# Optimization experiments

Measured on AMD Instinct MI355X. Metric: run time of the kernel, lower is better.

Reference implementation:

```python
import jax, jax.numpy as jnp
import numpy as np

VOCAB, VEC, HID, ATT, DOM, B, S = 50000, 300, 256, 500, 16, 64, 128


def _gru_scan(gi_all, h0, Whh, bhh):
    # gi_all: [S,B,3H] precomputed input projections; returns hs: [S,B,H]
    def step(h, gi):
        gh = h @ Whh.T + bhh
        i_r, i_z, i_n = jnp.split(gi, 3, axis=-1)
        h_r, h_z, h_n = jnp.split(gh, 3, axis=-1)
        r = jax.nn.sigmoid(i_r + h_r)
        zg = jax.nn.sigmoid(i_z + h_z)
        n = jnp.tanh(i_n + r * h_n)
        h_new = (1.0 - zg) * n + zg * h
        return h_new, h_new
    _, hs = jax.lax.scan(step, h0, gi_all)
    return hs


def setup_inputs() -> dict:
    key = jax.random.key(0)
    ks = jax.random.split(key, 16)
    def xavier(k, shape):
        fan_in, fan_out = shape[-1], shape[0]
        std = float(np.sqrt(2.0 / (fan_in + fan_out)))
        return jax.random.normal(k, shape, dtype=jnp.float32) * std
    inp = {
        'x': jax.random.randint(ks[0], (B, S), 0, VOCAB),
        'z': jax.random.randint(ks[1], (B,), 0, DOM),
        'emb': jax.random.normal(ks[2], (VOCAB, VEC), dtype=jnp.float32) * 0.1,
        'Wih_f': xavier(ks[3], (3 * HID, VEC)),
        'Whh_f': xavier(ks[4], (3 * HID, HID)),
        'bih_f': jnp.zeros((3 * HID,), jnp.float32),
        'bhh_f': jnp.zeros((3 * HID,), jnp.float32),
        'Wih_b': xavier(ks[5], (3 * HID, VEC)),
        'Whh_b': xavier(ks[6], (3 * HID, HID)),
        'bih_b': jnp.zeros((3 * HID,), jnp.float32),
        'bhh_b': jnp.zeros((3 * HID,), jnp.float32),
        'att_fc_W': xavier(ks[7], (ATT, 2 * HID)),
        'att_fc_b': jnp.zeros((ATT,), jnp.float32),
        'att_weight': xavier(ks[8], (DOM, ATT)),
        'fc_W': xavier(ks[9], (2, 2 * HID)),
        'fc_b': jnp.zeros((2,), jnp.float32),
    }
    return inp


def reference(x, z, emb, Wih_f, Whh_f, bih_f, bhh_f, Wih_b, Whh_b, bih_b, bhh_b,
              att_fc_W, att_fc_b, att_weight, fc_W, fc_b):
    xe = emb[x]                              # [B,S,VEC]
    xs = jnp.transpose(xe, (1, 0, 2))        # [S,B,VEC] (seq-major like torch GRU)
    h0 = jnp.zeros((x.shape[0], HID), jnp.float32)
    gi_f = jnp.einsum('sbv,gv->sbg', xs, Wih_f) + bih_f
    hs_f = _gru_scan(gi_f, h0, Whh_f, bhh_f)                       # [S,B,H]
    gi_b = jnp.einsum('sbv,gv->sbg', xs[::-1], Wih_b) + bih_b
    hs_b = _gru_scan(gi_b, h0, Whh_b, bhh_b)[::-1]                 # [S,B,H]
    h = jnp.transpose(jnp.concatenate([hs_f, hs_b], axis=-1), (1, 0, 2))  # [B,S,2H]
    hr = jnp.tanh(jnp.einsum('bsh,ah->bsa', h, att_fc_W) + att_fc_b)      # [B,S,ATT]
    # batched gather of per-domain attention vector, then per-row dot
    u = jnp.einsum('bsa,ba->bs', hr, att_weight[z])                        # [B,S]
    att = jax.nn.softmax(u, axis=1)                                        # [B,S]
    pooled = jnp.einsum('bsh,bs->bh', h, att)                              # [B,2H]
    # dropout is identity in eval mode
    return pooled @ fc_W.T + fc_b                                          # [B,2]
```

## Files before the change

### kernel.cpp

```cpp
#include <hip/hip_runtime.h>
#include <math.h>

#define VEC   300
#define HID   256
#define ATT   500
#define NB    64
#define NS    128
#define G3    768
#define GIC   1536
#define H2    512

typedef _Float16 half1;
typedef _Float16 h2_t  __attribute__((ext_vector_type(2)));
typedef _Float16 f16x8 __attribute__((ext_vector_type(8)));
typedef float    f32x4 __attribute__((ext_vector_type(4)));

struct __align__(16) H8 { h2_t a, b, c, d; };

#if __has_builtin(__builtin_amdgcn_exp2f)
#define EXP2F(x) __builtin_amdgcn_exp2f(x)
#else
#define EXP2F(x) exp2f(x)
#endif
#if __has_builtin(__builtin_amdgcn_rcpf)
#define RCPF(x) __builtin_amdgcn_rcpf(x)
#else
#define RCPF(x) (1.0f/(x))
#endif

__device__ __forceinline__ float sigm(float x){ return RCPF(1.f + EXP2F(-1.44269504f*x)); }
__device__ __forceinline__ float tanh_fast(float x){ return 1.f - 2.f*RCPF(1.f + EXP2F(2.88539008f*x)); }

#if __has_builtin(__builtin_amdgcn_fdot2)
#define FDOT(w,h,acc) __builtin_amdgcn_fdot2((w),(h),(acc),false)
#else
#define FDOT(w,h,acc) ((acc) + (float)(w).x*(float)(h).x + (float)(w).y*(float)(h).y)
#endif

__global__ __launch_bounds__(256) void k_prep(const float* __restrict__ Wf,
                       const float* __restrict__ Wb, h2_t* __restrict__ Wpk){
  int o = blockIdx.x*256 + threadIdx.x;
  int t = o & 1023;
  int rest = o >> 10;
  int j = rest % 3;
  int p = (rest/3) & 31;
  int dir = rest / 96;
  int u = t & 255, ks = t >> 8;
  const float* W = dir ? Wb : Wf;
  int k0 = ks*64 + 2*p;
  h2_t w;
  w.x = (half1)W[(j*HID+u)*HID + k0];
  w.y = (half1)W[(j*HID+u)*HID + k0 + 1];
  Wpk[o] = w;
}

__global__ __launch_bounds__(256) void k_prepA(const float* __restrict__ afW,
                       half1* __restrict__ afW16){
  int o = blockIdx.x*256 + threadIdx.x;
  int n = o >> 9, k = o & 511;
  afW16[o] = (half1)((n < ATT) ? afW[n*H2 + k] : 0.f);
}

__global__ __launch_bounds__(256)
__attribute__((amdgpu_waves_per_eu(4, 4)))
void k_gi_mfma(const int* __restrict__ x,
      const float* __restrict__ emb,
      const float* __restrict__ Wf, const float* __restrict__ Wb,
      const float* __restrict__ bf, const float* __restrict__ bb,
      float* __restrict__ gi){
  __shared__ half1 Al[128*40];
  __shared__ half1 Bl[128*40];
  __shared__ int   xi[128];
  const int t = threadIdx.x;
  const int row0 = blockIdx.x * 128;
  const int col0 = blockIdx.y * 128;
  if (t < 128) {
    int i = row0 + t; int s = i >> 6; int b = i & 63;
    xi[t] = x[b*NS + s];
  }
  __syncthreads();

  const int lane = t & 63, wid = t >> 6;
  const int wr = wid >> 1, wc = wid & 1;
  const int l15 = lane & 15, lk = lane >> 4;

  f32x4 acc[4][4];
#pragma unroll
  for (int i = 0; i < 4; ++i)
#pragma unroll
    for (int j = 0; j < 4; ++j) acc[i][j] = (f32x4){0.f,0.f,0.f,0.f};

  for (int ks = 0; ks < 10; ++ks) {
#pragma unroll
    for (int l = 0; l < 8; ++l) {
      int idx = l*256 + t;
      int row = idx >> 4;
      int kp  = idx & 15;
      int kk  = ks*32 + kp*2;
      h2_t va; va.x = (half1)0.f; va.y = (half1)0.f;
      h2_t vb; vb.x = (half1)0.f; vb.y = (half1)0.f;
      if (kk < VEC) {
        float2 e = *reinterpret_cast<const float2*>(&emb[(long)xi[row]*VEC + kk]);
        va.x = (half1)e.x; va.y = (half1)e.y;
        int g = col0 + row;
        const float* W = (g < G3) ? &Wf[(long)g*VEC] : &Wb[(long)(g-G3)*VEC];
        float2 w2 = *reinterpret_cast<const float2*>(&W[kk]);
        vb.x = (half1)w2.x; vb.y = (half1)w2.y;
      }
      *reinterpret_cast<h2_t*>(&Al[row*40 + kp*2]) = va;
      *reinterpret_cast<h2_t*>(&Bl[row*40 + kp*2]) = vb;
    }
    __syncthreads();
    f16x8 af[4], bfq[4];
#pragma unroll
    for (int i = 0; i < 4; ++i)
      af[i]  = *reinterpret_cast<const f16x8*>(&Al[(wr*64 + i*16 + l15)*40 + lk*8]);
#pragma unroll
    for (int j = 0; j < 4; ++j)
      bfq[j] = *reinterpret_cast<const f16x8*>(&Bl[(wc*64 + j*16 + l15)*40 + lk*8]);
#pragma unroll
    for (int i = 0; i < 4; ++i)
#pragma unroll
      for (int j = 0; j < 4; ++j)
        acc[i][j] = __builtin_amdgcn_mfma_f32_16x16x32_f16(af[i], bfq[j], acc[i][j], 0, 0, 0);
    __syncthreads();
  }

#pragma unroll
  for (int j = 0; j < 4; ++j) {
    int gcol = col0 + wc*64 + j*16 + l15;
    float bj = (gcol < G3) ? bf[gcol] : bb[gcol - G3];
#pragma unroll
    for (int i = 0; i < 4; ++i) {
      int grow0 = row0 + wr*64 + i*16 + lk*4;
#pragma unroll
      for (int q = 0; q < 4; ++q)
        gi[(long)(grow0 + q)*GIC + gcol] = acc[i][j][q] + bj;
    }
  }
}

#define DECL12(X,g,UNUSED) h2_t X##g##a0,X##g##a1,X##g##a2, X##g##b0,X##g##b1,X##g##b2, \
                                X##g##c0,X##g##c1,X##g##c2, X##g##d0,X##g##d1,X##g##d2;
#define LOAD12(X,g,WP) \
  X##g##a0=(WP)[((4*(g)+0)*3+0)*1024]; X##g##a1=(WP)[((4*(g)+0)*3+1)*1024]; X##g##a2=(WP)[((4*(g)+0)*3+2)*1024]; \
  X##g##b0=(WP)[((4*(g)+1)*3+0)*1024]; X##g##b1=(WP)[((4*(g)+1)*3+1)*1024]; X##g##b2=(WP)[((4*(g)+1)*3+2)*1024]; \
  X##g##c0=(WP)[((4*(g)+2)*3+0)*1024]; X##g##c1=(WP)[((4*(g)+2)*3+1)*1024]; X##g##c2=(WP)[((4*(g)+2)*3+2)*1024]; \
  X##g##d0=(WP)[((4*(g)+3)*3+0)*1024]; X##g##d1=(WP)[((4*(g)+3)*3+1)*1024]; X##g##d2=(WP)[((4*(g)+3)*3+2)*1024];
#define FMA12(X,g,BOFF) { \
  H8 hv = *reinterpret_cast<const H8*>(&hl16[kb + (BOFF) + (g)*8]); \
  a0=FDOT(X##g##a0,hv.a,a0); a1=FDOT(X##g##a1,hv.a,a1); a2=FDOT(X##g##a2,hv.a,a2); \
  a0=FDOT(X##g##b0,hv.b,a0); a1=FDOT(X##g##b1,hv.b,a1); a2=FDOT(X##g##b2,hv.b,a2); \
  a0=FDOT(X##g##c0,hv.c,a0); a1=FDOT(X##g##c1,hv.c,a1); a2=FDOT(X##g##c2,hv.c,a2); \
  a0=FDOT(X##g##d0,hv.d,a0); a1=FDOT(X##g##d1,hv.d,a1); a2=FDOT(X##g##d2,hv.d,a2); }
#define GRP8(M,X,A2) M(X,0,A2) M(X,1,A2) M(X,2,A2) M(X,3,A2) M(X,4,A2) M(X,5,A2) M(X,6,A2) M(X,7,A2)

__global__ __launch_bounds__(1024)
__attribute__((amdgpu_waves_per_eu(4, 4)))
void k_scan_reg3(const float* __restrict__ gi,
     const h2_t* __restrict__ Wpk,
     const float* __restrict__ bhf, const float* __restrict__ bhb,
     float* __restrict__ hseq){
  __shared__ __align__(16) half1 hl16[264];
  __shared__ float part[3*780];
  const int t   = threadIdx.x;
  const int u   = t & 255;
  const int ks  = t >> 8;
  const int kb  = ks * 64;
  const int dir = blockIdx.x & 1;
  const int b   = blockIdx.x >> 1;
  const float* bhh = dir ? bhb : bhf;
  const h2_t* wp = Wpk + (long)dir*96*1024 + t;

  GRP8(DECL12, A, 0)
  GRP8(LOAD12, A, wp)

  float bh0=0.f, bh1=0.f, bh2=0.f;
  if (ks == 0) { bh0 = bhh[u]; bh1 = bhh[HID+u]; bh2 = bhh[2*HID+u]; }
  if (t < 256) hl16[t] = (half1)0.f;
  float hprev = 0.f;

  const long gstep = dir ? -(long)NB*GIC : (long)NB*GIC;
  const long hstep = dir ? -(long)H2    : (long)H2;
  long gbase = ((long)(dir ? (NS-1) : 0)*NB + b)*GIC + dir*G3 + u;
  long hbase = ((long)b*NS + (dir ? (NS-1) : 0))*H2 + dir*HID + u;
  __syncthreads();

#pragma unroll 1
  for (int tt = 0; tt < NS; ++tt) {
    float i0=0.f, i1=0.f, i2=0.f;
    if (ks == 0) {
      i0 = gi[gbase]; i1 = gi[gbase+HID]; i2 = gi[gbase+2*HID];
    }
    float a0=0.f, a1=0.f, a2=0.f;
    GRP8(FMA12, A, 0)
    if (ks > 0) {
      float* p = &part[(ks-1)*780 + u];
      p[0] = a0; p[260] = a1; p[520] = a2;
    }
    __syncthreads();
    if (ks == 0) {
      float g0 = bh0 + a0 + part[u]     + part[780+u]     + part[1560+u];
      float g1 = bh1 + a1 + part[260+u] + part[1040+u]    + part[1820+u];
      float g2 = bh2 + a2 + part[520+u] + part[1300+u]    + part[2080+u];
      float r  = sigm(i0 + g0);
      float zg = sigm(i1 + g1);
      float n  = tanh_fast(i2 + r*g2);
      float hn = (1.f - zg)*n + zg*hprev;
      hprev = hn;
      hl16[u] = (half1)hn;
      hseq[hbase] = hn;
    }
    gbase += gstep; hbase += hstep;
    __syncthreads();
  }
}

__global__ __launch_bounds__(256)
__attribute__((amdgpu_waves_per_eu(4, 4)))
void k_att1_mfma(const float* __restrict__ hseq, const half1* __restrict__ afW16,
    const float* __restrict__ afb, const float* __restrict__ attw,
    const int* __restrict__ z, float* __restrict__ ub){
  __shared__ half1 Ah[32*520];
  __shared__ float red[4*32];
  const int t  = threadIdx.x;
  const int b  = blockIdx.x;
  const int s0 = blockIdx.y * 32;
  const int lane = t & 63, w = t >> 6;
  const int l15 = lane & 15, lk = lane >> 4;

#pragma unroll
  for (int l = 0; l < 64; ++l) {
    int idx = l*256 + t;
    int sl = idx >> 9, c = idx & 511;
    Ah[sl*520 + c] = (half1)hseq[((long)b*NS + s0 + sl)*H2 + c];
  }
  __syncthreads();

  f32x4 acc[2][8];
#pragma unroll
  for (int i = 0; i < 2; ++i)
#pragma unroll
    for (int j = 0; j < 8; ++j) acc[i][j] = (f32x4){0.f,0.f,0.f,0.f};

#pragma unroll 2
  for (int ksn = 0; ksn < 16; ++ksn) {
    f16x8 af[2];
#pragma unroll
    for (int mt = 0; mt < 2; ++mt)
      af[mt] = *reinterpret_cast<const f16x8*>(&Ah[(mt*16 + l15)*520 + ksn*32 + lk*8]);
#pragma unroll
    for (int nt = 0; nt < 8; ++nt) {
      int n = w*128 + nt*16 + l15;
      f16x8 bf = *reinterpret_cast<const f16x8*>(&afW16[(long)n*512 + ksn*32 + lk*8]);
#pragma unroll
      for (int mt = 0; mt < 2; ++mt)
        acc[mt][nt] = __builtin_amdgcn_mfma_f32_16x16x32_f16(af[mt], bf, acc[mt][nt], 0, 0, 0);
    }
  }

  float us[8];
#pragma unroll
  for (int i = 0; i < 8; ++i) us[i] = 0.f;
  const int zb = z[b];
#pragma unroll
  for (int nt = 0; nt < 8; ++nt) {
    int n = w*128 + nt*16 + l15;
    float ab = (n < ATT) ? afb[n] : 0.f;
    float aw = (n < ATT) ? attw[zb*ATT + n] : 0.f;
#pragma unroll
    for (int mt = 0; mt < 2; ++mt)
#pragma unroll
      for (int q = 0; q < 4; ++q)
        us[mt*4+q] += tanh_fast(acc[mt][nt][q] + ab) * aw;
  }
#pragma unroll
  for (int off = 1; off < 16; off <<= 1)
#pragma unroll
    for (int i = 0; i < 8; ++i) us[i] += __shfl_xor(us[i], off, 64);
  if (l15 == 0) {
#pragma unroll
    for (int i = 0; i < 8; ++i) {
      int row = (i >> 2)*16 + lk*4 + (i & 3);
      red[w*32 + row] = us[i];
    }
  }
  __syncthreads();
  if (t < 32)
    ub[b*NS + s0 + t] = red[t] + red[32+t] + red[64+t] + red[96+t];
}

__global__ __launch_bounds__(256) void k_att2(const float* __restrict__ hseq,
   const float* __restrict__ ub, const float* __restrict__ fcW,
   const float* __restrict__ fcb, float* __restrict__ out){
  __shared__ float att[NS];
  __shared__ float red[256];
  __shared__ float pool[H2];
  const int t = threadIdx.x, b = blockIdx.x;
  float v = (t < NS) ? ub[b*NS + t] : -3.4e38f;
  red[t] = v; __syncthreads();
  for (int off = 128; off >= 1; off >>= 1) {
    if (t < off) red[t] = fmaxf(red[t], red[t+off]);
    __syncthreads();
  }
  float mx = red[0]; __syncthreads();
  float e = (t < NS) ? EXP2F(1.44269504f*(v - mx)) : 0.f;
  red[t] = e; __syncthreads();
  for (int off = 128; off >= 1; off >>= 1) {
    if (t < off) red[t] += red[t+off];
    __syncthreads();
  }
  float sm = red[0]; __syncthreads();
  if (t < NS) att[t] = e / sm;
  __syncthreads();
#pragma unroll
  for (int rep = 0; rep < 2; ++rep) {
    int c = rep*256 + t;
    float acc = 0.f;
#pragma unroll 4
    for (int s = 0; s < NS; ++s) acc += att[s] * hseq[((long)b*NS + s)*H2 + c];
    pool[c] = acc;
  }
  __syncthreads();
  for (int j = 0; j < 2; ++j) {
    float p = pool[t]*fcW[j*H2+t] + pool[t+256]*fcW[j*H2+t+256];
    red[t] = p; __syncthreads();
    for (int off = 128; off >= 1; off >>= 1) {
      if (t < off) red[t] += red[t+off];
      __syncthreads();
    }
    if (t == 0) out[b*2+j] = red[0] + fcb[j];
    __syncthreads();
  }
}

extern "C" void kernel_launch(void* const* d_in, const int* in_sizes, int n_in,
                              void* d_out, int out_size, void* d_ws, size_t ws_size,
                              hipStream_t stream) {
  const int*   x     = (const int*)  d_in[0];
  const int*   z     = (const int*)  d_in[1];
  const float* emb   = (const float*)d_in[2];
  const float* Wih_f = (const float*)d_in[3];
  const float* Whh_f = (const float*)d_in[4];
  const float* bih_f = (const float*)d_in[5];
  const float* bhh_f = (const float*)d_in[6];
  const float* Wih_b = (const float*)d_in[7];
  const float* Whh_b = (const float*)d_in[8];
  const float* bih_b = (const float*)d_in[9];
  const float* bhh_b = (const float*)d_in[10];
  const float* afW   = (const float*)d_in[11];
  const float* afb   = (const float*)d_in[12];
  const float* attw  = (const float*)d_in[13];
  const float* fcW   = (const float*)d_in[14];
  const float* fcb   = (const float*)d_in[15];

  float* ws    = (float*)d_ws;
  h2_t*  Wpk   = (h2_t*)ws;
  half1* afW16 = (half1*)(ws + 196608);
  float* giW   = ws   + 196608 + 131072;
  float* hseq  = giW  + 12582912;
  float* ubuf  = hseq + 4194304;

  k_prep <<<dim3(768),  dim3(256), 0, stream>>>(Whh_f, Whh_b, Wpk);
  k_prepA<<<dim3(1024), dim3(256), 0, stream>>>(afW, afW16);
  k_gi_mfma<<<dim3(64,12), dim3(256), 0, stream>>>(x, emb, Wih_f, Wih_b, bih_f, bih_b, giW);
  k_scan_reg3<<<dim3(128), dim3(1024), 0, stream>>>(giW, Wpk, bhh_f, bhh_b, hseq);
  k_att1_mfma<<<dim3(64,4), dim3(256), 0, stream>>>(hseq, afW16, afb, attw, z, ubuf);
  k_att2<<<dim3(64), dim3(256), 0, stream>>>(hseq, ubuf, fcW, fcb, (float*)d_out);
}
```

Baseline: 249.3 us.

## Reduce GRU scan K-split partials with wave shuffles and double-buffer hidden state

The recurrent scan kernel's thread-to-work mapping changes so that the four K-slices of each hidden unit sit in the same wavefront. Partial dot products are then reduced with xor shuffles instead of a shared-memory partial buffer and an extra barrier. The hidden state is double-buffered in LDS with padded rows, so each timestep needs one __syncthreads instead of two. The weight-packing prep kernel is remapped to match the new layout. In exchange, each thread does six cross-lane shuffles per step, and only a quarter of the lanes compute the gate nonlinearities.

```diff
diff --git a/kernel.cpp b/kernel.cpp
--- a/kernel.cpp
+++ b/kernel.cpp
@@ -45,13 +45,14 @@
   int j = rest % 3;
   int p = (rest/3) & 31;
   int dir = rest / 96;
-  int u = t & 255, ks = t >> 8;
+  int ul = t & 15, ks = (t >> 4) & 3, w = t >> 6;
+  int u = w*16 + ul;
   const float* W = dir ? Wb : Wf;
   int k0 = ks*64 + 2*p;
-  h2_t w;
-  w.x = (half1)W[(j*HID+u)*HID + k0];
-  w.y = (half1)W[(j*HID+u)*HID + k0 + 1];
-  Wpk[o] = w;
+  h2_t wv;
+  wv.x = (half1)W[(j*HID+u)*HID + k0];
+  wv.y = (half1)W[(j*HID+u)*HID + k0 + 1];
+  Wpk[o] = wv;
 }
 
 __global__ __launch_bounds__(256) void k_prepA(const float* __restrict__ afW,
@@ -147,8 +148,8 @@
   X##g##b0=(WP)[((4*(g)+1)*3+0)*1024]; X##g##b1=(WP)[((4*(g)+1)*3+1)*1024]; X##g##b2=(WP)[((4*(g)+1)*3+2)*1024]; \
   X##g##c0=(WP)[((4*(g)+2)*3+0)*1024]; X##g##c1=(WP)[((4*(g)+2)*3+1)*1024]; X##g##c2=(WP)[((4*(g)+2)*3+2)*1024]; \
   X##g##d0=(WP)[((4*(g)+3)*3+0)*1024]; X##g##d1=(WP)[((4*(g)+3)*3+1)*1024]; X##g##d2=(WP)[((4*(g)+3)*3+2)*1024];
-#define FMA12(X,g,BOFF) { \
-  H8 hv = *reinterpret_cast<const H8*>(&hl16[kb + (BOFF) + (g)*8]); \
+#define FMA12(X,g,UNUSED) { \
+  H8 hv = *reinterpret_cast<const H8*>(&hl16r[kbp + (g)*8]); \
   a0=FDOT(X##g##a0,hv.a,a0); a1=FDOT(X##g##a1,hv.a,a1); a2=FDOT(X##g##a2,hv.a,a2); \
   a0=FDOT(X##g##b0,hv.b,a0); a1=FDOT(X##g##b1,hv.b,a1); a2=FDOT(X##g##b2,hv.b,a2); \
   a0=FDOT(X##g##c0,hv.c,a0); a1=FDOT(X##g##c1,hv.c,a1); a2=FDOT(X##g##c2,hv.c,a2); \
@@ -157,27 +158,30 @@
 
 __global__ __launch_bounds__(1024)
 __attribute__((amdgpu_waves_per_eu(4, 4)))
-void k_scan_reg3(const float* __restrict__ gi,
+void k_scan_reg4(const float* __restrict__ gi,
      const h2_t* __restrict__ Wpk,
      const float* __restrict__ bhf, const float* __restrict__ bhb,
      float* __restrict__ hseq){
-  __shared__ __align__(16) half1 hl16[264];
-  __shared__ float part[3*780];
-  const int t   = threadIdx.x;
-  const int u   = t & 255;
-  const int ks  = t >> 8;
-  const int kb  = ks * 64;
-  const int dir = blockIdx.x & 1;
-  const int b   = blockIdx.x >> 1;
+  __shared__ __align__(16) half1 hbuf[2][4*72];
+  const int t    = threadIdx.x;
+  const int lane = t & 63;
+  const int ul   = lane & 15;
+  const int ks   = lane >> 4;
+  const int w    = t >> 6;
+  const int u    = w*16 + ul;
+  const int kbp  = ks * 72;
+  const int dir  = blockIdx.x & 1;
+  const int b    = blockIdx.x >> 1;
   const float* bhh = dir ? bhb : bhf;
   const h2_t* wp = Wpk + (long)dir*96*1024 + t;
 
   GRP8(DECL12, A, 0)
   GRP8(LOAD12, A, wp)
 
+  const bool fin = (ks == 0);
   float bh0=0.f, bh1=0.f, bh2=0.f;
-  if (ks == 0) { bh0 = bhh[u]; bh1 = bhh[HID+u]; bh2 = bhh[2*HID+u]; }
-  if (t < 256) hl16[t] = (half1)0.f;
+  if (fin) { bh0 = bhh[u]; bh1 = bhh[HID+u]; bh2 = bhh[2*HID+u]; }
+  if (t < 288) hbuf[0][t] = (half1)0.f;
   float hprev = 0.f;
 
   const long gstep = dir ? -(long)NB*GIC : (long)NB*GIC;
@@ -188,27 +192,27 @@
 
 #pragma unroll 1
   for (int tt = 0; tt < NS; ++tt) {
+    const half1* hl16r = hbuf[tt & 1];
+    half1*       hl16w = hbuf[(tt + 1) & 1];
     float i0=0.f, i1=0.f, i2=0.f;
-    if (ks == 0) {
+    if (fin) {
       i0 = gi[gbase]; i1 = gi[gbase+HID]; i2 = gi[gbase+2*HID];
     }
     float a0=0.f, a1=0.f, a2=0.f;
     GRP8(FMA12, A, 0)
-    if (ks > 0) {
-      float* p = &part[(ks-1)*780 + u];
-      p[0] = a0; p[260] = a1; p[520] = a2;
-    }
-    __syncthreads();
-    if (ks == 0) {
-      float g0 = bh0 + a0 + part[u]     + part[780+u]     + part[1560+u];
-      float g1 = bh1 + a1 + part[260+u] + part[1040+u]    + part[1820+u];
-      float g2 = bh2 + a2 + part[520+u] + part[1300+u]    + part[2080+u];
+    a0 += __shfl_xor(a0, 16, 64); a0 += __shfl_xor(a0, 32, 64);
+    a1 += __shfl_xor(a1, 16, 64); a1 += __shfl_xor(a1, 32, 64);
+    a2 += __shfl_xor(a2, 16, 64); a2 += __shfl_xor(a2, 32, 64);
+    if (fin) {
+      float g0 = bh0 + a0;
+      float g1 = bh1 + a1;
+      float g2 = bh2 + a2;
       float r  = sigm(i0 + g0);
       float zg = sigm(i1 + g1);
       float n  = tanh_fast(i2 + r*g2);
       float hn = (1.f - zg)*n + zg*hprev;
       hprev = hn;
-      hl16[u] = (half1)hn;
+      hl16w[(u >> 6)*72 + (u & 63)] = (half1)hn;
       hseq[hbase] = hn;
     }
     gbase += gstep; hbase += hstep;
@@ -364,7 +368,7 @@
   k_prep <<<dim3(768),  dim3(256), 0, stream>>>(Whh_f, Whh_b, Wpk);
   k_prepA<<<dim3(1024), dim3(256), 0, stream>>>(afW, afW16);
   k_gi_mfma<<<dim3(64,12), dim3(256), 0, stream>>>(x, emb, Wih_f, Wih_b, bih_f, bih_b, giW);
-  k_scan_reg3<<<dim3(128), dim3(1024), 0, stream>>>(giW, Wpk, bhh_f, bhh_b, hseq);
+  k_scan_reg4<<<dim3(128), dim3(1024), 0, stream>>>(giW, Wpk, bhh_f, bhh_b, hseq);
   k_att1_mfma<<<dim3(64,4), dim3(256), 0, stream>>>(hseq, afW16, afb, attw, z, ubuf);
   k_att2<<<dim3(64), dim3(256), 0, stream>>>(hseq, ubuf, fcW, fcb, (float*)d_out);
 }
```

Result: slower. 257.5 us (+3.3%).
